# Optimization experiments

Measured on AMD Instinct MI355X. Metric: run time of the kernel, lower is better.

Reference implementation:

```python
import jax, jax.numpy as jnp
import numpy as np

N = 50000          # nodes
E = 1_600_000      # edges (avg degree 32)
IN = 16            # in_node_features
H0 = 64            # hidden_features_mlp[0]
D = 32             # hidden_features_mlp[1] == hidden_features_gnn
HF = 64            # hidden_final
OUT = 3            # out_features (congestion classes)
L = 3              # gnn_layer_num
EPS = 1e-5


def gelu(x):
    return jax.nn.gelu(x, approximate=False)  # torch nn.GELU default (erf)


def bn_eval(x, g, b):
    # BatchNorm1d in eval mode with fresh running stats (mean=0, var=1)
    return x * (g / jnp.sqrt(1.0 + EPS)) + b


def ln(x, g, b):
    m = jnp.mean(x, axis=-1, keepdims=True)
    v = jnp.var(x, axis=-1, keepdims=True)
    return (x - m) / jnp.sqrt(v + EPS) * g + b


def setup_inputs() -> dict:
    key = jax.random.key(0)
    ks = jax.random.split(key, 24)
    s = 0.1
    inp = {
        "x": jax.random.normal(ks[0], (N, IN), dtype=jnp.float32),
        "edge_index": jax.random.randint(ks[1], (2, E), 0, N, dtype=jnp.int32),
        # node_emb_mlp
        "emb_W1": jax.random.normal(ks[2], (IN, H0), dtype=jnp.float32) * s,
        "emb_b1": jnp.zeros((H0,), jnp.float32),
        "emb_bn1_g": jnp.ones((H0,), jnp.float32),
        "emb_bn1_b": jnp.zeros((H0,), jnp.float32),
        "emb_W2": jax.random.normal(ks[3], (H0, D), dtype=jnp.float32) * s,
        "emb_b2": jnp.zeros((D,), jnp.float32),
        "emb_bn2_g": jnp.ones((D,), jnp.float32),
        "emb_bn2_b": jnp.zeros((D,), jnp.float32),
        # GNN layers (stacked over L)
        "msg_W": jax.random.normal(ks[4], (L, 2 * D, D), dtype=jnp.float32) * s,
        "msg_b": jnp.zeros((L, D), jnp.float32),
        "msg_ln_g": jnp.ones((L, D), jnp.float32),
        "msg_ln_b": jnp.zeros((L, D), jnp.float32),
        "upd_W": jax.random.normal(ks[5], (L, 2 * D, D), dtype=jnp.float32) * s,
        "upd_b": jnp.zeros((L, D), jnp.float32),
        "upd_ln_g": jnp.ones((L, D), jnp.float32),
        "upd_ln_b": jnp.zeros((L, D), jnp.float32),
        # final_aggregation_layer
        "fin_W1": jax.random.normal(ks[6], (D, HF), dtype=jnp.float32) * s,
        "fin_b1": jnp.zeros((HF,), jnp.float32),
        "fin_bn_g": jnp.ones((HF,), jnp.float32),
        "fin_bn_b": jnp.zeros((HF,), jnp.float32),
        "fin_W2": jax.random.normal(ks[7], (HF, OUT), dtype=jnp.float32) * s,
        "fin_b2": jnp.zeros((OUT,), jnp.float32),
    }
    return inp


def reference(x, edge_index,
              emb_W1, emb_b1, emb_bn1_g, emb_bn1_b,
              emb_W2, emb_b2, emb_bn2_g, emb_bn2_b,
              msg_W, msg_b, msg_ln_g, msg_ln_b,
              upd_W, upd_b, upd_ln_g, upd_ln_b,
              fin_W1, fin_b1, fin_bn_g, fin_bn_b, fin_W2, fin_b2):
    src = edge_index[0]  # x_j (source, messages flow source->target)
    dst = edge_index[1]  # x_i (target, aggregation index)

    # node embedding MLP (dropout = identity in eval)
    h = gelu(bn_eval(x @ emb_W1 + emb_b1, emb_bn1_g, emb_bn1_b))
    h = gelu(bn_eval(h @ emb_W2 + emb_b2, emb_bn2_g, emb_bn2_b))
    pre = h

    for l in range(L):
        x_i = h[dst]  # [E, D]
        x_j = h[src]  # [E, D]
        m = gelu(ln(jnp.concatenate([x_i, x_j], axis=-1) @ msg_W[l] + msg_b[l],
                    msg_ln_g[l], msg_ln_b[l]))                 # [E, D]
        agg = jax.ops.segment_sum(m, dst, num_segments=N)      # [N, D]
        h = h + gelu(ln(jnp.concatenate([h, agg], axis=-1) @ upd_W[l] + upd_b[l],
                        upd_ln_g[l], upd_ln_b[l]))

    h = h + pre  # residual around the GNN stack

    general_emb = h[dst] - h[src]  # node_emb_j - node_emb_i, [E, D]
    out = gelu(bn_eval(general_emb @ fin_W1 + fin_b1, fin_bn_g, fin_bn_b))
    out = out @ fin_W2 + fin_b2  # [E, OUT] cc_scores
    return out
```

## Files before the change

kernel.cpp:

```cpp
#include <hip/hip_runtime.h>

#define NN 50000
#define NE 1600000
#define HIST_B 1563
#define EMB_B  782
constexpr float LN_EPS = 1e-5f;

typedef _Float16 half8 __attribute__((ext_vector_type(8)));

__device__ __forceinline__ float gelu_f(float x){
  float ax = fabsf(x) * 0.70710678118654752440f;
  float t  = __builtin_amdgcn_rcpf(fmaf(0.3275911f, ax, 1.0f));
  float e  = __expf(-ax*ax);
  float p  = t*fmaf(t, fmaf(t, fmaf(t, fmaf(t, 1.061405429f, -1.453152027f),
                                    1.421413741f), -0.284496736f), 0.254829592f);
  float er = fmaf(-p, e, 1.0f);
  return 0.5f * x * (1.0f + copysignf(er, x));
}

__device__ __forceinline__ void ld8(const float* __restrict__ p, float* r){
  float4 a=((const float4*)p)[0], b=((const float4*)p)[1];
  r[0]=a.x;r[1]=a.y;r[2]=a.z;r[3]=a.w;r[4]=b.x;r[5]=b.y;r[6]=b.z;r[7]=b.w;
}
__device__ __forceinline__ void ld16(const float* __restrict__ p, float* r){ ld8(p,r); ld8(p+8,r+8); }
__device__ __forceinline__ void st8(float* __restrict__ p, const float* r){
  float4 a,b; a.x=r[0];a.y=r[1];a.z=r[2];a.w=r[3]; b.x=r[4];b.y=r[5];b.z=r[6];b.w=r[7];
  ((float4*)p)[0]=a; ((float4*)p)[1]=b;
}

__global__ __launch_bounds__(256) void hist_embed_kernel(
    const int* __restrict__ ei, int* __restrict__ cnt, int* __restrict__ rank,
    const float* __restrict__ x,
    const float* __restrict__ W1, const float* __restrict__ b1,
    const float* __restrict__ g1, const float* __restrict__ bb1,
    const float* __restrict__ W2, const float* __restrict__ b2,
    const float* __restrict__ g2, const float* __restrict__ bb2,
    const float* __restrict__ Wm, const float* __restrict__ bm,
    const float* __restrict__ Wu, const float* __restrict__ bu,
    const float* __restrict__ fb1, const float* __restrict__ fbng, const float* __restrict__ fbnb,
    float* __restrict__ h, float* __restrict__ pre,
    float* __restrict__ P, _Float16* __restrict__ Qh, float* __restrict__ R,
    float* __restrict__ cvec)
{
  if(blockIdx.x < HIST_B){
    int t = blockIdx.x*256 + threadIdx.x;
    if(t < NE/4){
      int4 d = ((const int4*)(ei + NE))[t];
      int4 r;
      r.x = atomicAdd(&cnt[d.x],1);
      r.y = atomicAdd(&cnt[d.y],1);
      r.z = atomicAdd(&cnt[d.z],1);
      r.w = atomicAdd(&cnt[d.w],1);
      ((int4*)rank)[t] = r;
    }
    return;
  }
  int t = (blockIdx.x - HIST_B)*256 + threadIdx.x;
  const float rs = rsqrtf(1.0f + LN_EPS);
  if(t < 64) cvec[t] = fmaf(fb1[t], fbng[t]*rs, fbnb[t]);
  int n = t >> 2, q = t & 3;
  if(n >= NN) return;
  int base = threadIdx.x & 60;
  float4 xq = ((const float4*)x)[n*4 + q];
  float xv[16];
  #pragma unroll
  for(int m=0;m<4;m++){
    xv[4*m+0]=__shfl(xq.x, base|m);
    xv[4*m+1]=__shfl(xq.y, base|m);
    xv[4*m+2]=__shfl(xq.z, base|m);
    xv[4*m+3]=__shfl(xq.w, base|m);
  }
  float a1q[16]; ld16(b1 + q*16, a1q);
  #pragma unroll
  for(int k=0;k<16;k++){
    float w[16]; ld16(W1 + k*64 + q*16, w);
    float xk = xv[k];
    #pragma unroll
    for(int j=0;j<16;j++) a1q[j] += xk * w[j];
  }
  { float g[16], b[16]; ld16(g1+q*16,g); ld16(bb1+q*16,b);
    #pragma unroll
    for(int j=0;j<16;j++) a1q[j] = gelu_f(a1q[j]*(g[j]*rs) + b[j]); }
  float hq[8]; ld8(b2 + q*8, hq);
  #pragma unroll
  for(int m=0;m<4;m++){
    #pragma unroll
    for(int kk=0;kk<16;kk++){
      float a = __shfl(a1q[kk], base|m);
      float w[8]; ld8(W2 + (m*16+kk)*32 + q*8, w);
      #pragma unroll
      for(int j=0;j<8;j++) hq[j] += a * w[j];
    }
  }
  { float g[8], b[8]; ld8(g2+q*8,g); ld8(bb2+q*8,b);
    #pragma unroll
    for(int j=0;j<8;j++) hq[j] = gelu_f(hq[j]*(g[j]*rs) + b[j]); }
  st8(h   + (size_t)n*32 + q*8, hq);
  st8(pre + (size_t)n*32 + q*8, hq);
  float apv[8], aqv[8], arv[8];
  ld8(bm+q*8, apv); ld8(bu+q*8, arv);
  #pragma unroll
  for(int j=0;j<8;j++) aqv[j]=0.f;
  #pragma unroll
  for(int m=0;m<4;m++){
    #pragma unroll
    for(int kk=0;kk<8;kk++){
      float hk = __shfl(hq[kk], base|m);
      int k = m*8+kk;
      float wm[8],wq[8],wu[8];
      ld8(Wm + k*32      + q*8, wm);
      ld8(Wm + (32+k)*32 + q*8, wq);
      ld8(Wu + k*32      + q*8, wu);
      #pragma unroll
      for(int j=0;j<8;j++){ apv[j]+=hk*wm[j]; aqv[j]+=hk*wq[j]; arv[j]+=hk*wu[j]; }
    }
  }
  st8(P + (size_t)n*32 + q*8, apv);
  st8(R + (size_t)n*32 + q*8, arv);
  half8 qo;
  #pragma unroll
  for(int k=0;k<8;k++) qo[k] = (_Float16)aqv[k];
  *(half8*)(Qh + (size_t)n*32 + q*8) = qo;
}

#define CHUNK 52
__global__ __launch_bounds__(1024) void scan_kernel(const int* __restrict__ deg, int* __restrict__ row_ptr){
  __shared__ int sums[1024];
  int t = threadIdx.x;
  int base = t*CHUNK;
  int4 v[13];
  int ssum = 0;
  #pragma unroll
  for(int i=0;i<13;i++){
    int idx = base + 4*i;
    if(idx + 3 < NN){
      v[i] = ((const int4*)deg)[(base>>2)+i];
    } else {
      v[i].x = (idx+0<NN)?deg[idx+0]:0; v[i].y = (idx+1<NN)?deg[idx+1]:0;
      v[i].z = (idx+2<NN)?deg[idx+2]:0; v[i].w = (idx+3<NN)?deg[idx+3]:0;
    }
    ssum += v[i].x + v[i].y + v[i].z + v[i].w;
  }
  sums[t]=ssum;
  __syncthreads();
  for(int off=1; off<1024; off<<=1){
    int vv = (t>=off) ? sums[t-off] : 0;
    __syncthreads();
    sums[t] += vv;
    __syncthreads();
  }
  int run = (t>0) ? sums[t-1] : 0;
  #pragma unroll
  for(int i=0;i<13;i++){
    int idx = base + 4*i;
    int4 o;
    o.x = run; run += v[i].x;
    o.y = run; run += v[i].y;
    o.z = run; run += v[i].z;
    o.w = run; run += v[i].w;
    if(idx + 3 < NN){
      ((int4*)row_ptr)[(base>>2)+i] = o;
    } else {
      if(idx+0<NN) row_ptr[idx+0]=o.x;
      if(idx+1<NN) row_ptr[idx+1]=o.y;
      if(idx+2<NN) row_ptr[idx+2]=o.z;
      if(idx+3<NN) row_ptr[idx+3]=o.w;
    }
  }
  if(t==1023) row_ptr[NN] = sums[1023];
}

__global__ __launch_bounds__(256) void fill_kernel(const int* __restrict__ ei,
    const int* __restrict__ row_ptr, const int* __restrict__ rank, int* __restrict__ csr_src){
  int t = blockIdx.x*256 + threadIdx.x;
  if(t < NE/4){
    int4 d  = ((const int4*)(ei + NE))[t];
    int4 sv = ((const int4*)ei)[t];
    int4 rk = ((const int4*)rank)[t];
    csr_src[row_ptr[d.x] + rk.x] = sv.x;
    csr_src[row_ptr[d.y] + rk.y] = sv.y;
    csr_src[row_ptr[d.z] + rk.z] = sv.z;
    csr_src[row_ptr[d.w] + rk.w] = sv.w;
  }
}

__global__ __launch_bounds__(256) void msg_kernel(
    const float* __restrict__ P, const _Float16* __restrict__ Qh,
    const int* __restrict__ row_ptr, const int* __restrict__ csr_src,
    const float* __restrict__ mg, const float* __restrict__ mb,
    float* __restrict__ aggO)
{
  int tid = blockIdx.x*256 + threadIdx.x;
  int n = tid >> 4;
  int s = tid & 15;
  int slot = s >> 2;
  int q = s & 3;
  float mgq[8], mbq[8], p8[8];
  ld8(mg + q*8, mgq); ld8(mb + q*8, mbq);
  ld8(P + (size_t)n*32 + q*8, p8);
  float agg8[8] = {0,0,0,0,0,0,0,0};
  int e0 = row_ptr[n], e1 = row_ptr[n+1];
  int e = e0 + slot;
  int src = (e < e1) ? csr_src[e] : 0;
  half8 qv = *(const half8*)(Qh + (size_t)src*32 + q*8);
  while(e < e1){
    int e2 = e + 4;
    int src2 = (e2 < e1) ? csr_src[e2] : 0;
    half8 qv2 = *(const half8*)(Qh + (size_t)src2*32 + q*8);
    float v[8];
    #pragma unroll
    for(int k=0;k<8;k++) v[k] = p8[k] + (float)qv[k];
    float ps = ((v[0]+v[1])+(v[2]+v[3])) + ((v[4]+v[5])+(v[6]+v[7]));
    ps += __shfl_xor(ps,1); ps += __shfl_xor(ps,2);
    float mean = ps * 0.03125f;
    float vs = 0.f;
    #pragma unroll
    for(int k=0;k<8;k++){ float dd = v[k]-mean; vs += dd*dd; v[k]=dd; }
    vs += __shfl_xor(vs,1); vs += __shfl_xor(vs,2);
    float rstd = rsqrtf(vs*0.03125f + LN_EPS);
    #pragma unroll
    for(int k=0;k<8;k++) agg8[k] += gelu_f(v[k]*rstd*mgq[k] + mbq[k]);
    qv = qv2; e = e2;
  }
  #pragma unroll
  for(int k=0;k<8;k++) agg8[k] += __shfl_xor(agg8[k], 4);
  #pragma unroll
  for(int k=0;k<8;k++) agg8[k] += __shfl_xor(agg8[k], 8);
  if(slot==0) st8(aggO + (size_t)n*32 + q*8, agg8);
}

__global__ __launch_bounds__(256) void upd_pqr_kernel(
    const float* __restrict__ aggI, const float* __restrict__ Rio,
    const float* __restrict__ Ub,
    const float* __restrict__ ug, const float* __restrict__ ub,
    const float* __restrict__ Wm2, const float* __restrict__ bm2,
    const float* __restrict__ Wu2, const float* __restrict__ bu2,
    float* __restrict__ h,
    float* __restrict__ P, _Float16* __restrict__ Qh, float* __restrict__ Rout)
{
  int t = blockIdx.x*256 + threadIdx.x;
  int n = t >> 2, q = t & 3;
  if(n >= NN) return;
  int base = threadIdx.x & 60;
  float aggq[8], uq[8];
  ld8(aggI + (size_t)n*32 + q*8, aggq);
  ld8(Rio  + (size_t)n*32 + q*8, uq);
  #pragma unroll
  for(int m=0;m<4;m++){
    #pragma unroll
    for(int kk=0;kk<8;kk++){
      float a = __shfl(aggq[kk], base|m);
      float w[8]; ld8(Ub + (m*8+kk)*32 + q*8, w);
      #pragma unroll
      for(int j=0;j<8;j++) uq[j] += a * w[j];
    }
  }
  float sm = ((uq[0]+uq[1])+(uq[2]+uq[3])) + ((uq[4]+uq[5])+(uq[6]+uq[7]));
  sm += __shfl_xor(sm,1); sm += __shfl_xor(sm,2);
  float mean = sm * 0.03125f;
  float vs = 0.f;
  #pragma unroll
  for(int j=0;j<8;j++){ float d = uq[j]-mean; vs += d*d; uq[j]=d; }
  vs += __shfl_xor(vs,1); vs += __shfl_xor(vs,2);
  float rstd = rsqrtf(vs*0.03125f + LN_EPS);
  float ugq[8], ubq[8], hq[8];
  ld8(ug+q*8, ugq); ld8(ub+q*8, ubq);
  ld8(h + (size_t)n*32 + q*8, hq);
  #pragma unroll
  for(int j=0;j<8;j++) hq[j] += gelu_f(uq[j]*rstd*ugq[j] + ubq[j]);
  st8(h + (size_t)n*32 + q*8, hq);
  float apv[8], aqv[8], arv[8];
  ld8(bm2+q*8, apv); ld8(bu2+q*8, arv);
  #pragma unroll
  for(int j=0;j<8;j++) aqv[j]=0.f;
  #pragma unroll
  for(int m=0;m<4;m++){
    #pragma unroll
    for(int kk=0;kk<8;kk++){
      float hk = __shfl(hq[kk], base|m);
      int k = m*8+kk;
      float wm[8],wq[8],wu[8];
      ld8(Wm2 + k*32      + q*8, wm);
      ld8(Wm2 + (32+k)*32 + q*8, wq);
      ld8(Wu2 + k*32      + q*8, wu);
      #pragma unroll
      for(int j=0;j<8;j++){ apv[j]+=hk*wm[j]; aqv[j]+=hk*wq[j]; arv[j]+=hk*wu[j]; }
    }
  }
  st8(P    + (size_t)n*32 + q*8, apv);
  st8(Rout + (size_t)n*32 + q*8, arv);
  half8 qo;
  #pragma unroll
  for(int k=0;k<8;k++) qo[k] = (_Float16)aqv[k];
  *(half8*)(Qh + (size_t)n*32 + q*8) = qo;
}

__global__ __launch_bounds__(256) void upd_fin_kernel(
    const float* __restrict__ aggI, const float* __restrict__ Rio,
    const float* __restrict__ Ub,
    const float* __restrict__ ug, const float* __restrict__ ub,
    const float* __restrict__ h, const float* __restrict__ pre,
    const float* __restrict__ fW1, const float* __restrict__ fbng,
    _Float16* __restrict__ y1, _Float16* __restrict__ y2)
{
  int t = blockIdx.x*256 + threadIdx.x;
  int n = t >> 2, q = t & 3;
  if(n >= NN) return;
  int base = threadIdx.x & 60;
  const float rs = rsqrtf(1.0f + LN_EPS);
  float aggq[8], uq[8];
  ld8(aggI + (size_t)n*32 + q*8, aggq);
  ld8(Rio  + (size_t)n*32 + q*8, uq);
  #pragma unroll
  for(int m=0;m<4;m++){
    #pragma unroll
    for(int kk=0;kk<8;kk++){
      float a = __shfl(aggq[kk], base|m);
      float w[8]; ld8(Ub + (m*8+kk)*32 + q*8, w);
      #pragma unroll
      for(int j=0;j<8;j++) uq[j] += a * w[j];
    }
  }
  float sm = ((uq[0]+uq[1])+(uq[2]+uq[3])) + ((uq[4]+uq[5])+(uq[6]+uq[7]));
  sm += __shfl_xor(sm,1); sm += __shfl_xor(sm,2);
  float mean = sm * 0.03125f;
  float vs = 0.f;
  #pragma unroll
  for(int j=0;j<8;j++){ float d = uq[j]-mean; vs += d*d; uq[j]=d; }
  vs += __shfl_xor(vs,1); vs += __shfl_xor(vs,2);
  float rstd = rsqrtf(vs*0.03125f + LN_EPS);
  float ugq[8], ubq[8], hq[8], pq[8];
  ld8(ug+q*8, ugq); ld8(ub+q*8, ubq);
  ld8(h   + (size_t)n*32 + q*8, hq);
  ld8(pre + (size_t)n*32 + q*8, pq);
  #pragma unroll
  for(int j=0;j<8;j++) hq[j] += gelu_f(uq[j]*rstd*ugq[j] + ubq[j]) + pq[j];
  float acc[16];
  #pragma unroll
  for(int j=0;j<16;j++) acc[j]=0.f;
  #pragma unroll
  for(int m=0;m<4;m++){
    #pragma unroll
    for(int kk=0;kk<8;kk++){
      float hk = __shfl(hq[kk], base|m);
      float w[16]; ld16(fW1 + (m*8+kk)*64 + q*16, w);
      #pragma unroll
      for(int j=0;j<16;j++) acc[j] += hk * w[j];
    }
  }
  float fg[16]; ld16(fbng + q*16, fg);
  half8 o0, o1;
  #pragma unroll
  for(int k=0;k<8;k++){
    o0[k] = (_Float16)(acc[k]   * (fg[k]*rs));
    o1[k] = (_Float16)(acc[8+k] * (fg[8+k]*rs));
  }
  _Float16* dst = (q<2) ? (y1 + (size_t)n*32 + q*16) : (y2 + (size_t)n*32 + (q-2)*16);
  ((half8*)dst)[0] = o0; ((half8*)dst)[1] = o1;
}

__global__ __launch_bounds__(256) void finalA_kernel(
    const _Float16* __restrict__ y, const int* __restrict__ ei,
    const float* __restrict__ cvec, const float* __restrict__ W2,
    const float* __restrict__ b2, float* __restrict__ out)
{
  int t = blockIdx.x*256 + threadIdx.x;
  int e = t >> 2, q = t & 3;
  int s = __builtin_nontemporal_load(ei + e);
  int d = __builtin_nontemporal_load(ei + NE + e);
  half8 a8 = *(const half8*)(y + (size_t)d*32 + q*8);
  half8 c8 = *(const half8*)(y + (size_t)s*32 + q*8);
  float cq[8]; ld8(cvec + q*8, cq);
  float w[24]; ld8(W2+q*24, w); ld8(W2+q*24+8, w+8); ld8(W2+q*24+16, w+16);
  float o0=0.f,o1=0.f,o2=0.f;
  #pragma unroll
  for(int k=0;k<8;k++){
    float tt = gelu_f(((float)a8[k]-(float)c8[k]) + cq[k]);
    o0 += tt*w[3*k]; o1 += tt*w[3*k+1]; o2 += tt*w[3*k+2];
  }
  o0 += __shfl_xor(o0,1); o0 += __shfl_xor(o0,2);
  o1 += __shfl_xor(o1,1); o1 += __shfl_xor(o1,2);
  o2 += __shfl_xor(o2,1); o2 += __shfl_xor(o2,2);
  float ov = (q==0) ? o0 + b2[0] : (q==1) ? o1 + b2[1] : o2 + b2[2];
  if(q < 3) __builtin_nontemporal_store(ov, out + (size_t)e*3 + q);
}

__global__ __launch_bounds__(256) void finalB_kernel(
    const _Float16* __restrict__ y, const int* __restrict__ ei,
    const float* __restrict__ cvec, const float* __restrict__ W2,
    float* __restrict__ out)
{
  int t = blockIdx.x*256 + threadIdx.x;
  int e = t >> 2, q = t & 3;
  float prev = 0.f;
  if(q < 3) prev = __builtin_nontemporal_load(out + (size_t)e*3 + q);
  int s = __builtin_nontemporal_load(ei + e);
  int d = __builtin_nontemporal_load(ei + NE + e);
  half8 a8 = *(const half8*)(y + (size_t)d*32 + q*8);
  half8 c8 = *(const half8*)(y + (size_t)s*32 + q*8);
  float cq[8]; ld8(cvec + q*8, cq);
  float w[24]; ld8(W2+q*24, w); ld8(W2+q*24+8, w+8); ld8(W2+q*24+16, w+16);
  float o0=0.f,o1=0.f,o2=0.f;
  #pragma unroll
  for(int k=0;k<8;k++){
    float tt = gelu_f(((float)a8[k]-(float)c8[k]) + cq[k]);
    o0 += tt*w[3*k]; o1 += tt*w[3*k+1]; o2 += tt*w[3*k+2];
  }
  o0 += __shfl_xor(o0,1); o0 += __shfl_xor(o0,2);
  o1 += __shfl_xor(o1,1); o1 += __shfl_xor(o1,2);
  o2 += __shfl_xor(o2,1); o2 += __shfl_xor(o2,2);
  float ov = prev + ((q==0) ? o0 : (q==1) ? o1 : o2);
  if(q < 3) __builtin_nontemporal_store(ov, out + (size_t)e*3 + q);
}

extern "C" void kernel_launch(void* const* d_in, const int* in_sizes, int n_in,
                              void* d_out, int out_size, void* d_ws, size_t ws_size,
                              hipStream_t stream)
{
  (void)in_sizes; (void)n_in; (void)out_size; (void)ws_size;
  const float* x     = (const float*)d_in[0];
  const int*   ei    = (const int*)d_in[1];
  const float* eW1   = (const float*)d_in[2];
  const float* eb1   = (const float*)d_in[3];
  const float* ebn1g = (const float*)d_in[4];
  const float* ebn1b = (const float*)d_in[5];
  const float* eW2   = (const float*)d_in[6];
  const float* eb2   = (const float*)d_in[7];
  const float* ebn2g = (const float*)d_in[8];
  const float* ebn2b = (const float*)d_in[9];
  const float* msgW  = (const float*)d_in[10];
  const float* msgb  = (const float*)d_in[11];
  const float* msglng= (const float*)d_in[12];
  const float* msglnb= (const float*)d_in[13];
  const float* updW  = (const float*)d_in[14];
  const float* updb  = (const float*)d_in[15];
  const float* updlng= (const float*)d_in[16];
  const float* updlnb= (const float*)d_in[17];
  const float* fW1   = (const float*)d_in[18];
  const float* fb1   = (const float*)d_in[19];
  const float* fbng  = (const float*)d_in[20];
  const float* fbnb  = (const float*)d_in[21];
  const float* fW2   = (const float*)d_in[22];
  const float* fb2   = (const float*)d_in[23];
  float* out = (float*)d_out;

  float* f   = (float*)d_ws;
  float* h   = f;
  float* pre = f + 1*(size_t)NN*32;
  float* P   = f + 2*(size_t)NN*32;
  float* R   = f + 3*(size_t)NN*32;
  float* agg = f + 4*(size_t)NN*32;
  _Float16* Qh = (_Float16*)(f + 5*(size_t)NN*32);
  _Float16* y1 = (_Float16*)P;
  _Float16* y2 = y1 + (size_t)NN*32;
  float* cvec  = f + 5*(size_t)NN*32 + (size_t)NN*16;
  int* ip      = (int*)(cvec + 64);
  int* cnt     = ip;
  int* row_ptr = ip + NN;
  int* csr     = ip + 2*NN + 4;
  int* rank    = (int*)agg;

  hipMemsetAsync(cnt, 0, NN*sizeof(int), stream);
  hist_embed_kernel<<<HIST_B + EMB_B, 256, 0, stream>>>(ei, cnt, rank,
      x, eW1, eb1, ebn1g, ebn1b, eW2, eb2, ebn2g, ebn2b,
      msgW, msgb, updW, updb,
      fb1, fbng, fbnb,
      h, pre, P, Qh, R, cvec);
  scan_kernel<<<1, 1024, 0, stream>>>(cnt, row_ptr);
  fill_kernel<<<HIST_B, 256, 0, stream>>>(ei, row_ptr, rank, csr);

  for(int l=0; l<3; l++){
    msg_kernel<<<(NN*16)/256, 256, 0, stream>>>(P, Qh, row_ptr, csr,
        msglng + l*32, msglnb + l*32, agg);
    if(l < 2){
      upd_pqr_kernel<<<EMB_B, 256, 0, stream>>>(agg, R,
          updW + l*2048 + 1024, updlng + l*32, updlnb + l*32,
          msgW + (l+1)*2048, msgb + (l+1)*32,
          updW + (l+1)*2048, updb + (l+1)*32,
          h, P, Qh, R);
    } else {
      upd_fin_kernel<<<EMB_B, 256, 0, stream>>>(agg, R,
          updW + l*2048 + 1024, updlng + l*32, updlnb + l*32,
          h, pre, fW1, fbng, y1, y2);
    }
  }

  finalA_kernel<<<(NE*4)/256, 256, 0, stream>>>(y1, ei, cvec,      fW2,      fb2, out);
  finalB_kernel<<<(NE*4)/256, 256, 0, stream>>>(y2, ei, cvec + 32, fW2 + 96, out);
}
```

Measured before the change: 517.1 us.

## Fuse message aggregation with node update per layer using double-buffered Q

```diff
diff --git a/kernel.cpp b/kernel.cpp
--- a/kernel.cpp
+++ b/kernel.cpp
@@ -2,8 +2,9 @@
 
 #define NN 50000
 #define NE 1600000
-#define HIST_B 1563
+#define FILL_B 1563
 #define EMB_B  782
+#define HIST_STRIDE 100096
 constexpr float LN_EPS = 1e-5f;
 
 typedef _Float16 half8 __attribute__((ext_vector_type(8)));
@@ -28,99 +29,28 @@
   ((float4*)p)[0]=a; ((float4*)p)[1]=b;
 }
 
-__global__ __launch_bounds__(256) void hist_embed_kernel(
-    const int* __restrict__ ei, int* __restrict__ cnt, int* __restrict__ rank,
-    const float* __restrict__ x,
-    const float* __restrict__ W1, const float* __restrict__ b1,
-    const float* __restrict__ g1, const float* __restrict__ bb1,
-    const float* __restrict__ W2, const float* __restrict__ b2,
-    const float* __restrict__ g2, const float* __restrict__ bb2,
-    const float* __restrict__ Wm, const float* __restrict__ bm,
-    const float* __restrict__ Wu, const float* __restrict__ bu,
-    const float* __restrict__ fb1, const float* __restrict__ fbng, const float* __restrict__ fbnb,
-    float* __restrict__ h, float* __restrict__ pre,
-    float* __restrict__ P, _Float16* __restrict__ Qh, float* __restrict__ R,
-    float* __restrict__ cvec)
-{
-  if(blockIdx.x < HIST_B){
-    int t = blockIdx.x*256 + threadIdx.x;
-    if(t < NE/4){
-      int4 d = ((const int4*)(ei + NE))[t];
-      int4 r;
-      r.x = atomicAdd(&cnt[d.x],1);
-      r.y = atomicAdd(&cnt[d.y],1);
-      r.z = atomicAdd(&cnt[d.z],1);
-      r.w = atomicAdd(&cnt[d.w],1);
-      ((int4*)rank)[t] = r;
-    }
-    return;
-  }
-  int t = (blockIdx.x - HIST_B)*256 + threadIdx.x;
-  const float rs = rsqrtf(1.0f + LN_EPS);
-  if(t < 64) cvec[t] = fmaf(fb1[t], fbng[t]*rs, fbnb[t]);
-  int n = t >> 2, q = t & 3;
-  if(n >= NN) return;
-  int base = threadIdx.x & 60;
-  float4 xq = ((const float4*)x)[n*4 + q];
-  float xv[16];
-  #pragma unroll
-  for(int m=0;m<4;m++){
-    xv[4*m+0]=__shfl(xq.x, base|m);
-    xv[4*m+1]=__shfl(xq.y, base|m);
-    xv[4*m+2]=__shfl(xq.z, base|m);
-    xv[4*m+3]=__shfl(xq.w, base|m);
-  }
-  float a1q[16]; ld16(b1 + q*16, a1q);
-  #pragma unroll
-  for(int k=0;k<16;k++){
-    float w[16]; ld16(W1 + k*64 + q*16, w);
-    float xk = xv[k];
-    #pragma unroll
-    for(int j=0;j<16;j++) a1q[j] += xk * w[j];
-  }
-  { float g[16], b[16]; ld16(g1+q*16,g); ld16(bb1+q*16,b);
-    #pragma unroll
-    for(int j=0;j<16;j++) a1q[j] = gelu_f(a1q[j]*(g[j]*rs) + b[j]); }
-  float hq[8]; ld8(b2 + q*8, hq);
-  #pragma unroll
-  for(int m=0;m<4;m++){
-    #pragma unroll
-    for(int kk=0;kk<16;kk++){
-      float a = __shfl(a1q[kk], base|m);
-      float w[8]; ld8(W2 + (m*16+kk)*32 + q*8, w);
-      #pragma unroll
-      for(int j=0;j<8;j++) hq[j] += a * w[j];
-    }
-  }
-  { float g[8], b[8]; ld8(g2+q*8,g); ld8(bb2+q*8,b);
-    #pragma unroll
-    for(int j=0;j<8;j++) hq[j] = gelu_f(hq[j]*(g[j]*rs) + b[j]); }
-  st8(h   + (size_t)n*32 + q*8, hq);
-  st8(pre + (size_t)n*32 + q*8, hq);
-  float apv[8], aqv[8], arv[8];
-  ld8(bm+q*8, apv); ld8(bu+q*8, arv);
-  #pragma unroll
-  for(int j=0;j<8;j++) aqv[j]=0.f;
-  #pragma unroll
-  for(int m=0;m<4;m++){
-    #pragma unroll
-    for(int kk=0;kk<8;kk++){
-      float hk = __shfl(hq[kk], base|m);
-      int k = m*8+kk;
-      float wm[8],wq[8],wu[8];
-      ld8(Wm + k*32      + q*8, wm);
-      ld8(Wm + (32+k)*32 + q*8, wq);
-      ld8(Wu + k*32      + q*8, wu);
-      #pragma unroll
-      for(int j=0;j<8;j++){ apv[j]+=hk*wm[j]; aqv[j]+=hk*wq[j]; arv[j]+=hk*wu[j]; }
-    }
-  }
-  st8(P + (size_t)n*32 + q*8, apv);
-  st8(R + (size_t)n*32 + q*8, arv);
-  half8 qo;
-  #pragma unroll
-  for(int k=0;k<8;k++) qo[k] = (_Float16)aqv[k];
-  *(half8*)(Qh + (size_t)n*32 + q*8) = qo;
+__global__ __launch_bounds__(256) void hist_kernel(const int* __restrict__ ei,
+    int* __restrict__ cnt, int* __restrict__ rank){
+  int t = blockIdx.x*256 + threadIdx.x;
+  int i0 = t, i1 = t + HIST_STRIDE, i2 = t + 2*HIST_STRIDE, i3 = t + 3*HIST_STRIDE;
+  bool v0 = i0 < NE/4, v1 = i1 < NE/4, v2 = i2 < NE/4, v3 = i3 < NE/4;
+  int4 d0 = v0 ? ((const int4*)(ei + NE))[i0] : make_int4(0,0,0,0);
+  int4 d1 = v1 ? ((const int4*)(ei + NE))[i1] : make_int4(0,0,0,0);
+  int4 d2 = v2 ? ((const int4*)(ei + NE))[i2] : make_int4(0,0,0,0);
+  int4 d3 = v3 ? ((const int4*)(ei + NE))[i3] : make_int4(0,0,0,0);
+  int4 r0, r1, r2, r3;
+  if(v0){ r0.x = atomicAdd(&cnt[d0.x],1); r0.y = atomicAdd(&cnt[d0.y],1);
+          r0.z = atomicAdd(&cnt[d0.z],1); r0.w = atomicAdd(&cnt[d0.w],1); }
+  if(v1){ r1.x = atomicAdd(&cnt[d1.x],1); r1.y = atomicAdd(&cnt[d1.y],1);
+          r1.z = atomicAdd(&cnt[d1.z],1); r1.w = atomicAdd(&cnt[d1.w],1); }
+  if(v2){ r2.x = atomicAdd(&cnt[d2.x],1); r2.y = atomicAdd(&cnt[d2.y],1);
+          r2.z = atomicAdd(&cnt[d2.z],1); r2.w = atomicAdd(&cnt[d2.w],1); }
+  if(v3){ r3.x = atomicAdd(&cnt[d3.x],1); r3.y = atomicAdd(&cnt[d3.y],1);
+          r3.z = atomicAdd(&cnt[d3.z],1); r3.w = atomicAdd(&cnt[d3.w],1); }
+  if(v0) ((int4*)rank)[i0] = r0;
+  if(v1) ((int4*)rank)[i1] = r1;
+  if(v2) ((int4*)rank)[i2] = r2;
+  if(v3) ((int4*)rank)[i3] = r3;
 }
 
 #define CHUNK 52
@@ -184,29 +114,106 @@
   }
 }
 
-__global__ __launch_bounds__(256) void msg_kernel(
-    const float* __restrict__ P, const _Float16* __restrict__ Qh,
+__global__ __launch_bounds__(256) void embed_pqr_kernel(
+    const float* __restrict__ x,
+    const float* __restrict__ W1, const float* __restrict__ b1,
+    const float* __restrict__ g1, const float* __restrict__ bb1,
+    const float* __restrict__ W2, const float* __restrict__ b2,
+    const float* __restrict__ g2, const float* __restrict__ bb2,
+    const float* __restrict__ Wm, const float* __restrict__ bm,
+    const float* __restrict__ Wu, const float* __restrict__ bu,
+    const float* __restrict__ fb1, const float* __restrict__ fbng, const float* __restrict__ fbnb,
+    float* __restrict__ h, float* __restrict__ pre,
+    float* __restrict__ P, _Float16* __restrict__ Qh, float* __restrict__ R,
+    float* __restrict__ cvec)
+{
+  int t = blockIdx.x*256 + threadIdx.x;
+  const float rs = rsqrtf(1.0f + LN_EPS);
+  if(t < 64) cvec[t] = fmaf(fb1[t], fbng[t]*rs, fbnb[t]);
+  int n = t >> 2, q = t & 3;
+  if(n >= NN) return;
+  int base = threadIdx.x & 60;
+  float4 xq = ((const float4*)x)[n*4 + q];
+  float xv[16];
+  #pragma unroll
+  for(int m=0;m<4;m++){
+    xv[4*m+0]=__shfl(xq.x, base|m);
+    xv[4*m+1]=__shfl(xq.y, base|m);
+    xv[4*m+2]=__shfl(xq.z, base|m);
+    xv[4*m+3]=__shfl(xq.w, base|m);
+  }
+  float a1q[16]; ld16(b1 + q*16, a1q);
+  #pragma unroll
+  for(int k=0;k<16;k++){
+    float w[16]; ld16(W1 + k*64 + q*16, w);
+    float xk = xv[k];
+    #pragma unroll
+    for(int j=0;j<16;j++) a1q[j] += xk * w[j];
+  }
+  { float g[16], b[16]; ld16(g1+q*16,g); ld16(bb1+q*16,b);
+    #pragma unroll
+    for(int j=0;j<16;j++) a1q[j] = gelu_f(a1q[j]*(g[j]*rs) + b[j]); }
+  float hq[8]; ld8(b2 + q*8, hq);
+  #pragma unroll
+  for(int m=0;m<4;m++){
+    #pragma unroll
+    for(int kk=0;kk<16;kk++){
+      float a = __shfl(a1q[kk], base|m);
+      float w[8]; ld8(W2 + (m*16+kk)*32 + q*8, w);
+      #pragma unroll
+      for(int j=0;j<8;j++) hq[j] += a * w[j];
+    }
+  }
+  { float g[8], b[8]; ld8(g2+q*8,g); ld8(bb2+q*8,b);
+    #pragma unroll
+    for(int j=0;j<8;j++) hq[j] = gelu_f(hq[j]*(g[j]*rs) + b[j]); }
+  st8(h   + (size_t)n*32 + q*8, hq);
+  st8(pre + (size_t)n*32 + q*8, hq);
+  float apv[8], aqv[8], arv[8];
+  ld8(bm+q*8, apv); ld8(bu+q*8, arv);
+  #pragma unroll
+  for(int j=0;j<8;j++) aqv[j]=0.f;
+  #pragma unroll
+  for(int m=0;m<4;m++){
+    #pragma unroll
+    for(int kk=0;kk<8;kk++){
+      float hk = __shfl(hq[kk], base|m);
+      int k = m*8+kk;
+      float wm[8],wq[8],wu[8];
+      ld8(Wm + k*32      + q*8, wm);
+      ld8(Wm + (32+k)*32 + q*8, wq);
+      ld8(Wu + k*32      + q*8, wu);
+      #pragma unroll
+      for(int j=0;j<8;j++){ apv[j]+=hk*wm[j]; aqv[j]+=hk*wq[j]; arv[j]+=hk*wu[j]; }
+    }
+  }
+  st8(P + (size_t)n*32 + q*8, apv);
+  st8(R + (size_t)n*32 + q*8, arv);
+  half8 qo;
+  #pragma unroll
+  for(int k=0;k<8;k++) qo[k] = (_Float16)aqv[k];
+  *(half8*)(Qh + (size_t)n*32 + q*8) = qo;
+}
+
+__device__ __forceinline__ void msg_gather(
+    const float* __restrict__ P, const _Float16* __restrict__ Qin,
     const int* __restrict__ row_ptr, const int* __restrict__ csr_src,
     const float* __restrict__ mg, const float* __restrict__ mb,
-    float* __restrict__ aggO)
-{
-  int tid = blockIdx.x*256 + threadIdx.x;
-  int n = tid >> 4;
-  int s = tid & 15;
-  int slot = s >> 2;
-  int q = s & 3;
+    int n, int slot, int q, float* agg8)
+{
   float mgq[8], mbq[8], p8[8];
   ld8(mg + q*8, mgq); ld8(mb + q*8, mbq);
   ld8(P + (size_t)n*32 + q*8, p8);
-  float agg8[8] = {0,0,0,0,0,0,0,0};
+  #pragma unroll
+  for(int k=0;k<8;k++) agg8[k]=0.f;
   int e0 = row_ptr[n], e1 = row_ptr[n+1];
   int e = e0 + slot;
   int src = (e < e1) ? csr_src[e] : 0;
-  half8 qv = *(const half8*)(Qh + (size_t)src*32 + q*8);
+  half8 qv = *(const half8*)(Qin + (size_t)src*32 + q*8);
   while(e < e1){
     int e2 = e + 4;
     int src2 = (e2 < e1) ? csr_src[e2] : 0;
-    half8 qv2 = *(const half8*)(Qh + (size_t)src2*32 + q*8);
+    half8 qv2 = *(const half8*)(Qin + (size_t)src2*32 + q*8);
     float v[8];
     #pragma unroll
     for(int k=0;k<8;k++) v[k] = p8[k] + (float)qv[k];
@@ -226,49 +233,59 @@
   for(int k=0;k<8;k++) agg8[k] += __shfl_xor(agg8[k], 4);
   #pragma unroll
   for(int k=0;k<8;k++) agg8[k] += __shfl_xor(agg8[k], 8);
-  if(slot==0) st8(aggO + (size_t)n*32 + q*8, agg8);
-}
-
-__global__ __launch_bounds__(256) void upd_pqr_kernel(
-    const float* __restrict__ aggI, const float* __restrict__ Rio,
+}
+
+__device__ __forceinline__ void upd_tail(
+    const float* __restrict__ R, float* __restrict__ h,
+    const float* __restrict__ Ub, const float* __restrict__ ug, const float* __restrict__ ub,
+    int n, int slot, int q, int b4, const float* agg8, float* hq)
+{
+  float uq[8]; ld8(R + (size_t)n*32 + q*8, uq);
+  #pragma unroll
+  for(int m=0;m<4;m++){
+    #pragma unroll
+    for(int kk=0;kk<8;kk++){
+      float a = __shfl(agg8[kk], b4|m);
+      float w[8]; ld8(Ub + (m*8+kk)*32 + q*8, w);
+      #pragma unroll
+      for(int j=0;j<8;j++) uq[j] += a * w[j];
+    }
+  }
+  float sm = ((uq[0]+uq[1])+(uq[2]+uq[3])) + ((uq[4]+uq[5])+(uq[6]+uq[7]));
+  sm += __shfl_xor(sm,1); sm += __shfl_xor(sm,2);
+  float mean = sm * 0.03125f;
+  float vs = 0.f;
+  #pragma unroll
+  for(int j=0;j<8;j++){ float d = uq[j]-mean; vs += d*d; uq[j]=d; }
+  vs += __shfl_xor(vs,1); vs += __shfl_xor(vs,2);
+  float rstd = rsqrtf(vs*0.03125f + LN_EPS);
+  float ugq[8], ubq[8];
+  ld8(ug+q*8, ugq); ld8(ub+q*8, ubq);
+  ld8(h + (size_t)n*32 + q*8, hq);
+  #pragma unroll
+  for(int j=0;j<8;j++) hq[j] += gelu_f(uq[j]*rstd*ugq[j] + ubq[j]);
+  if(slot==0) st8(h + (size_t)n*32 + q*8, hq);
+}
+
+__global__ __launch_bounds__(256) void msg_upd_kernel(
+    float* __restrict__ P, const _Float16* __restrict__ Qin,
+    float* __restrict__ R, float* __restrict__ h,
+    const int* __restrict__ row_ptr, const int* __restrict__ csr_src,
+    const float* __restrict__ mg, const float* __restrict__ mb,
     const float* __restrict__ Ub,
     const float* __restrict__ ug, const float* __restrict__ ub,
     const float* __restrict__ Wm2, const float* __restrict__ bm2,
     const float* __restrict__ Wu2, const float* __restrict__ bu2,
-    float* __restrict__ h,
-    float* __restrict__ P, _Float16* __restrict__ Qh, float* __restrict__ Rout)
-{
-  int t = blockIdx.x*256 + threadIdx.x;
-  int n = t >> 2, q = t & 3;
-  if(n >= NN) return;
-  int base = threadIdx.x & 60;
-  float aggq[8], uq[8];
-  ld8(aggI + (size_t)n*32 + q*8, aggq);
-  ld8(Rio  + (size_t)n*32 + q*8, uq);
-  #pragma unroll
-  for(int m=0;m<4;m++){
-    #pragma unroll
-    for(int kk=0;kk<8;kk++){
-      float a = __shfl(aggq[kk], base|m);
-      float w[8]; ld8(Ub + (m*8+kk)*32 + q*8, w);
-      #pragma unroll
-      for(int j=0;j<8;j++) uq[j] += a * w[j];
-    }
-  }
-  float sm = ((uq[0]+uq[1])+(uq[2]+uq[3])) + ((uq[4]+uq[5])+(uq[6]+uq[7]));
-  sm += __shfl_xor(sm,1); sm += __shfl_xor(sm,2);
-  float mean = sm * 0.03125f;
-  float vs = 0.f;
-  #pragma unroll
-  for(int j=0;j<8;j++){ float d = uq[j]-mean; vs += d*d; uq[j]=d; }
-  vs += __shfl_xor(vs,1); vs += __shfl_xor(vs,2);
-  float rstd = rsqrtf(vs*0.03125f + LN_EPS);
-  float ugq[8], ubq[8], hq[8];
-  ld8(ug+q*8, ugq); ld8(ub+q*8, ubq);
-  ld8(h + (size_t)n*32 + q*8, hq);
-  #pragma unroll
-  for(int j=0;j<8;j++) hq[j] += gelu_f(uq[j]*rstd*ugq[j] + ubq[j]);
-  st8(h + (size_t)n*32 + q*8, hq);
+    _Float16* __restrict__ Qout)
+{
+  int tid = blockIdx.x*256 + threadIdx.x;
+  int n = tid >> 4, s = tid & 15;
+  int slot = s >> 2, q = s & 3;
+  int b4 = (threadIdx.x & 63) & 60;
+  float agg8[8];
+  msg_gather(P, Qin, row_ptr, csr_src, mg, mb, n, slot, q, agg8);
+  float hq[8];
+  upd_tail(R, h, Ub, ug, ub, n, slot, q, b4, agg8, hq);
   float apv[8], aqv[8], arv[8];
   ld8(bm2+q*8, apv); ld8(bu2+q*8, arv);
   #pragma unroll
@@ -277,7 +294,7 @@
   for(int m=0;m<4;m++){
     #pragma unroll
     for(int kk=0;kk<8;kk++){
-      float hk = __shfl(hq[kk], base|m);
+      float hk = __shfl(hq[kk], b4|m);
       int k = m*8+kk;
       float wm[8],wq[8],wu[8];
       ld8(Wm2 + k*32      + q*8, wm);
@@ -287,76 +304,63 @@
       for(int j=0;j<8;j++){ apv[j]+=hk*wm[j]; aqv[j]+=hk*wq[j]; arv[j]+=hk*wu[j]; }
     }
   }
-  st8(P    + (size_t)n*32 + q*8, apv);
-  st8(Rout + (size_t)n*32 + q*8, arv);
-  half8 qo;
-  #pragma unroll
-  for(int k=0;k<8;k++) qo[k] = (_Float16)aqv[k];
-  *(half8*)(Qh + (size_t)n*32 + q*8) = qo;
-}
-
-__global__ __launch_bounds__(256) void upd_fin_kernel(
-    const float* __restrict__ aggI, const float* __restrict__ Rio,
+  if(slot==0){
+    st8(P + (size_t)n*32 + q*8, apv);
+    st8(R + (size_t)n*32 + q*8, arv);
+    half8 qo;
+    #pragma unroll
+    for(int k=0;k<8;k++) qo[k] = (_Float16)aqv[k];
+    *(half8*)(Qout + (size_t)n*32 + q*8) = qo;
+  }
+}
+
+__global__ __launch_bounds__(256) void msg_fin_kernel(
+    float* __restrict__ P, const _Float16* __restrict__ Qin,
+    float* __restrict__ R, float* __restrict__ h,
+    const int* __restrict__ row_ptr, const int* __restrict__ csr_src,
+    const float* __restrict__ mg, const float* __restrict__ mb,
     const float* __restrict__ Ub,
     const float* __restrict__ ug, const float* __restrict__ ub,
-    const float* __restrict__ h, const float* __restrict__ pre,
+    const float* __restrict__ pre,
     const float* __restrict__ fW1, const float* __restrict__ fbng,
     _Float16* __restrict__ y1, _Float16* __restrict__ y2)
 {
-  int t = blockIdx.x*256 + threadIdx.x;
-  int n = t >> 2, q = t & 3;
-  if(n >= NN) return;
-  int base = threadIdx.x & 60;
+  int tid = blockIdx.x*256 + threadIdx.x;
+  int n = tid >> 4, s = tid & 15;
+  int slot = s >> 2, q = s & 3;
+  int b4 = (threadIdx.x & 63) & 60;
   const float rs = rsqrtf(1.0f + LN_EPS);
-  float aggq[8], uq[8];
-  ld8(aggI + (size_t)n*32 + q*8, aggq);
-  ld8(Rio  + (size_t)n*32 + q*8, uq);
+  float agg8[8];
+  msg_gather(P, Qin, row_ptr, csr_src, mg, mb, n, slot, q, agg8);
+  float hq[8];
+  upd_tail(R, h, Ub, ug, ub, n, slot, q, b4, agg8, hq);
+  float pq[8]; ld8(pre + (size_t)n*32 + q*8, pq);
+  #pragma unroll
+  for(int j=0;j<8;j++) hq[j] += pq[j];
+  float acc[16];
+  #pragma unroll
+  for(int j=0;j<16;j++) acc[j]=0.f;
   #pragma unroll
   for(int m=0;m<4;m++){
     #pragma unroll
     for(int kk=0;kk<8;kk++){
-      float a = __shfl(aggq[kk], base|m);
-      float w[8]; ld8(Ub + (m*8+kk)*32 + q*8, w);
-      #pragma unroll
-      for(int j=0;j<8;j++) uq[j] += a * w[j];
-    }
-  }
-  float sm = ((uq[0]+uq[1])+(uq[2]+uq[3])) + ((uq[4]+uq[5])+(uq[6]+uq[7]));
-  sm += __shfl_xor(sm,1); sm += __shfl_xor(sm,2);
-  float mean = sm * 0.03125f;
-  float vs = 0.f;
-  #pragma unroll
-  for(int j=0;j<8;j++){ float d = uq[j]-mean; vs += d*d; uq[j]=d; }
-  vs += __shfl_xor(vs,1); vs += __shfl_xor(vs,2);
-  float rstd = rsqrtf(vs*0.03125f + LN_EPS);
-  float ugq[8], ubq[8], hq[8], pq[8];
-  ld8(ug+q*8, ugq); ld8(ub+q*8, ubq);
-  ld8(h   + (size_t)n*32 + q*8, hq);
-  ld8(pre + (size_t)n*32 + q*8, pq);
-  #pragma unroll
-  for(int j=0;j<8;j++) hq[j] += gelu_f(uq[j]*rstd*ugq[j] + ubq[j]) + pq[j];
-  float acc[16];
-  #pragma unroll
-  for(int j=0;j<16;j++) acc[j]=0.f;
-  #pragma unroll
-  for(int m=0;m<4;m++){
-    #pragma unroll
-    for(int kk=0;kk<8;kk++){
-      float hk = __shfl(hq[kk], base|m);
+      float hk = __shfl(hq[kk], b4|m);
       float w[16]; ld16(fW1 + (m*8+kk)*64 + q*16, w);
       #pragma unroll
       for(int j=0;j<16;j++) acc[j] += hk * w[j];
     }
   }
-  float fg[16]; ld16(fbng + q*16, fg);
-  half8 o0, o1;
-  #pragma unroll
-  for(int k=0;k<8;k++){
-    o0[k] = (_Float16)(acc[k]   * (fg[k]*rs));
-    o1[k] = (_Float16)(acc[8+k] * (fg[8+k]*rs));
-  }
-  _Float16* dst = (q<2) ? (y1 + (size_t)n*32 + q*16) : (y2 + (size_t)n*32 + (q-2)*16);
-  ((half8*)dst)[0] = o0; ((half8*)dst)[1] = o1;
+  if(slot==0){
+    float fg[16]; ld16(fbng + q*16, fg);
+    half8 o0, o1;
+    #pragma unroll
+    for(int k=0;k<8;k++){
+      o0[k] = (_Float16)(acc[k]   * (fg[k]*rs));
+      o1[k] = (_Float16)(acc[8+k] * (fg[8+k]*rs));
+    }
+    _Float16* dst = (q<2) ? (y1 + (size_t)n*32 + q*16) : (y2 + (size_t)n*32 + (q-2)*16);
+    ((half8*)dst)[0] = o0; ((half8*)dst)[1] = o1;
+  }
 }
 
 __global__ __launch_bounds__(256) void finalA_kernel(
@@ -449,41 +453,43 @@
   float* pre = f + 1*(size_t)NN*32;
   float* P   = f + 2*(size_t)NN*32;
   float* R   = f + 3*(size_t)NN*32;
-  float* agg = f + 4*(size_t)NN*32;
-  _Float16* Qh = (_Float16*)(f + 5*(size_t)NN*32);
-  _Float16* y1 = (_Float16*)P;
-  _Float16* y2 = y1 + (size_t)NN*32;
-  float* cvec  = f + 5*(size_t)NN*32 + (size_t)NN*16;
+  float* QAf = f + 4*(size_t)NN*32;
+  float* QBf = QAf + (size_t)NN*16;
+  float* y2f = QBf + (size_t)NN*16;
+  _Float16* QA = (_Float16*)QAf;
+  _Float16* QB = (_Float16*)QBf;
+  _Float16* y1 = (_Float16*)QBf;
+  _Float16* y2 = (_Float16*)y2f;
+  float* cvec  = y2f + (size_t)NN*16;
   int* ip      = (int*)(cvec + 64);
   int* cnt     = ip;
   int* row_ptr = ip + NN;
   int* csr     = ip + 2*NN + 4;
-  int* rank    = (int*)agg;
+  int* rank    = (int*)h;
 
   hipMemsetAsync(cnt, 0, NN*sizeof(int), stream);
-  hist_embed_kernel<<<HIST_B + EMB_B, 256, 0, stream>>>(ei, cnt, rank,
-      x, eW1, eb1, ebn1g, ebn1b, eW2, eb2, ebn2g, ebn2b,
+  hist_kernel<<<391, 256, 0, stream>>>(ei, cnt, rank);
+  scan_kernel<<<1, 1024, 0, stream>>>(cnt, row_ptr);
+  fill_kernel<<<FILL_B, 256, 0, stream>>>(ei, row_ptr, rank, csr);
+
+  embed_pqr_kernel<<<EMB_B, 256, 0, stream>>>(x, eW1, eb1, ebn1g, ebn1b,
+      eW2, eb2, ebn2g, ebn2b,
       msgW, msgb, updW, updb,
       fb1, fbng, fbnb,
-      h, pre, P, Qh, R, cvec);
-  scan_kernel<<<1, 1024, 0, stream>>>(cnt, row_ptr);
-  fill_kernel<<<HIST_B, 256, 0, stream>>>(ei, row_ptr, rank, csr);
-
-  for(int l=0; l<3; l++){
-    msg_kernel<<<(NN*16)/256, 256, 0, stream>>>(P, Qh, row_ptr, csr,
-        msglng + l*32, msglnb + l*32, agg);
-    if(l < 2){
-      upd_pqr_kernel<<<EMB_B, 256, 0, stream>>>(agg, R,
-          updW + l*2048 + 1024, updlng + l*32, updlnb + l*32,
-          msgW + (l+1)*2048, msgb + (l+1)*32,
-          updW + (l+1)*2048, updb + (l+1)*32,
-          h, P, Qh, R);
-    } else {
-      upd_fin_kernel<<<EMB_B, 256, 0, stream>>>(agg, R,
-          updW + l*2048 + 1024, updlng + l*32, updlnb + l*32,
-          h, pre, fW1, fbng, y1, y2);
-    }
-  }
+      h, pre, P, QA, R, cvec);
+
+  msg_upd_kernel<<<(NN*16)/256, 256, 0, stream>>>(P, QA, R, h, row_ptr, csr,
+      msglng + 0*32, msglnb + 0*32,
+      updW + 0*2048 + 1024, updlng + 0*32, updlnb + 0*32,
+      msgW + 1*2048, msgb + 1*32, updW + 1*2048, updb + 1*32, QB);
+  msg_upd_kernel<<<(NN*16)/256, 256, 0, stream>>>(P, QB, R, h, row_ptr, csr,
+      msglng + 1*32, msglnb + 1*32,
+      updW + 1*2048 + 1024, updlng + 1*32, updlnb + 1*32,
+      msgW + 2*2048, msgb + 2*32, updW + 2*2048, updb + 2*32, QA);
+  msg_fin_kernel<<<(NN*16)/256, 256, 0, stream>>>(P, QA, R, h, row_ptr, csr,
+      msglng + 2*32, msglnb + 2*32,
+      updW + 2*2048 + 1024, updlng + 2*32, updlnb + 2*32,
+      pre, fW1, fbng, y1, y2);
 
   finalA_kernel<<<(NE*4)/256, 256, 0, stream>>>(y1, ei, cvec,      fW2,      fb2, out);
   finalB_kernel<<<(NE*4)/256, 256, 0, stream>>>(y2, ei, cvec + 32, fW2 + 96, out);
```

Measured after the change: 801.2 us. 55.0% more time.
